# Kernel optimization log

Measured on AMD Instinct MI355X. Metric: run time of the kernel, lower is better.

The kernel has to match this reference:

```python
import jax, jax.numpy as jnp
import numpy as np
import math

N_HEAD = 8
LN_EPS = 1e-5


def _layernorm(x, w, b):
    # Biased variance as in the triton kernel: var = E[x^2] - mean^2
    mean = jnp.mean(x, axis=-1, keepdims=True)
    var = jnp.mean(x * x, axis=-1, keepdims=True) - mean * mean
    return (x - mean) * jax.lax.rsqrt(var + LN_EPS) * w + b


def _gelu_tanh(x):
    # matches triton gelu: tanh approximation
    return 0.5 * x * (1.0 + jnp.tanh(0.7978845608 * (x + 0.044715 * x * x * x)))


def _causal_attention(qkv, n_head):
    B, T, C3 = qkv.shape
    C = C3 // 3
    D = C // n_head
    q, k, v = jnp.split(qkv, 3, axis=-1)
    q = q.reshape(B, T, n_head, D)
    k = k.reshape(B, T, n_head, D)
    v = v.reshape(B, T, n_head, D)
    scale = 1.0 / math.sqrt(D)
    scores = jnp.einsum('bqhd,bkhd->bhqk', q, k) * scale  # [B,H,T,T]
    causal = jnp.tril(jnp.ones((T, T), dtype=bool))
    scores = jnp.where(causal, scores, -jnp.inf)
    p = jax.nn.softmax(scores, axis=-1)
    out = jnp.einsum('bhqk,bkhd->bqhd', p, v)
    return out.reshape(B, T, C)


def setup_inputs() -> dict:
    key = jax.random.key(0)
    ks = jax.random.split(key, 8)
    B, T, C = 8, 2048, 768
    s = 0.02
    return {
        'x': jax.random.normal(ks[0], (B, T, C), jnp.float32),
        'ln1_w': jnp.ones((C,), jnp.float32),
        'ln1_b': jnp.zeros((C,), jnp.float32),
        'w_qkv': jax.random.normal(ks[1], (3 * C, C), jnp.float32) * s,
        'b_qkv': jnp.zeros((3 * C,), jnp.float32),
        'w_attn_proj': jax.random.normal(ks[2], (C, C), jnp.float32) * s,
        'b_attn_proj': jnp.zeros((C,), jnp.float32),
        'ln2_w': jnp.ones((C,), jnp.float32),
        'ln2_b': jnp.zeros((C,), jnp.float32),
        'w_fc': jax.random.normal(ks[3], (4 * C, C), jnp.float32) * s,
        'b_fc': jnp.zeros((4 * C,), jnp.float32),
        'w_mlp_proj': jax.random.normal(ks[4], (C, 4 * C), jnp.float32) * s,
        'b_mlp_proj': jnp.zeros((C,), jnp.float32),
    }


def reference(x, ln1_w, ln1_b, w_qkv, b_qkv, w_attn_proj, b_attn_proj,
              ln2_w, ln2_b, w_fc, b_fc, w_mlp_proj, b_mlp_proj):
    # attention block: fused LN + QKV linear, causal flash attention, out proj, residual
    qkv = _layernorm(x, ln1_w, ln1_b) @ w_qkv.T + b_qkv          # [B,T,3C]
    att = _causal_attention(qkv, N_HEAD)                          # [B,T,C]
    x = x + (att @ w_attn_proj.T + b_attn_proj)
    # MLP block: fused LN + fc + gelu, proj, residual
    h = _gelu_tanh(_layernorm(x, ln2_w, ln2_b) @ w_fc.T + b_fc)   # [B,T,4C]
    x = x + (h @ w_mlp_proj.T + b_mlp_proj)
    return x
```

## Files before the change

kernel.cpp:

```cpp
#include <hip/hip_runtime.h>
#include <hip/hip_bf16.h>
#include <cstdint>
#include <cstddef>

typedef __attribute__((ext_vector_type(8))) short bf16x8;
typedef __attribute__((ext_vector_type(4))) short bf16x4;
typedef __attribute__((ext_vector_type(4))) float f32x4;
typedef __attribute__((ext_vector_type(16))) float f32x16;

#define GLB_AS(p) ((const __attribute__((address_space(1))) void*)(p))
#define LDS_AS(p) ((__attribute__((address_space(3))) void*)(p))

__device__ __forceinline__ short f2bf(float f) {
    union { float f; unsigned u; } x; x.f = f;
    unsigned r = (x.u + 0x7fffu + ((x.u >> 16) & 1u)) >> 16;
    return (short)r;
}
__device__ __forceinline__ unsigned packbf2(float a, float b) {
    union { float f; unsigned u; } x, y; x.f = a; y.f = b;
    return (x.u >> 16) | (y.u & 0xffff0000u);
}
__device__ __forceinline__ f32x4 MF(bf16x8 a, bf16x8 b, f32x4 c) {
    return __builtin_amdgcn_mfma_f32_16x16x32_bf16(a, b, c, 0, 0, 0);
}
__device__ __forceinline__ f32x16 MF32(bf16x8 a, bf16x8 b, f32x16 c) {
    return __builtin_amdgcn_mfma_f32_32x32x16_bf16(a, b, c, 0, 0, 0);
}

__global__ __launch_bounds__(256) void k_cast4(const float* __restrict__ s0,
                                               const float* __restrict__ s1,
                                               const float* __restrict__ s2,
                                               const float* __restrict__ s3,
                                               short* __restrict__ d0,
                                               short* __restrict__ d1,
                                               short* __restrict__ d2,
                                               short* __restrict__ d3,
                                               int n0, int n1, int n2, int n3) {
    const int total = n0 + n1 + n2 + n3;
    int i = blockIdx.x * 256 + threadIdx.x;
    const int stride = gridDim.x * 256;
    for (; i < total; i += stride) {
        int j = i;
        const float* s; short* d;
        if (j < n0) { s = s0; d = d0; }
        else {
            j -= n0;
            if (j < n1) { s = s1; d = d1; }
            else {
                j -= n1;
                if (j < n2) { s = s2; d = d2; }
                else { j -= n2; s = s3; d = d3; }
            }
        }
        float4 v = ((const float4*)s)[j];
        bf16x4 o;
        o[0] = f2bf(v.x); o[1] = f2bf(v.y); o[2] = f2bf(v.z); o[3] = f2bf(v.w);
        ((bf16x4*)d)[j] = o;
    }
}

__global__ __launch_bounds__(256) void k_layernorm(const float* __restrict__ x,
                                                   const float* __restrict__ w,
                                                   const float* __restrict__ b,
                                                   short* __restrict__ out) {
    const int row = blockIdx.x;
    const int tid = threadIdx.x;
    const float* xr = x + (size_t)row * 768;
    float v0 = xr[tid], v1 = xr[tid + 256], v2 = xr[tid + 512];
    float s = v0 + v1 + v2;
    float ss = v0 * v0 + v1 * v1 + v2 * v2;
    #pragma unroll
    for (int m = 32; m; m >>= 1) { s += __shfl_xor(s, m); ss += __shfl_xor(ss, m); }
    __shared__ float red[8];
    int wid = tid >> 6, lane = tid & 63;
    if (lane == 0) { red[wid] = s; red[4 + wid] = ss; }
    __syncthreads();
    s = red[0] + red[1] + red[2] + red[3];
    ss = red[4] + red[5] + red[6] + red[7];
    float mean = s * (1.f / 768.f);
    float var = ss * (1.f / 768.f) - mean * mean;
    float inv = rsqrtf(var + 1e-5f);
    short* orow = out + (size_t)row * 768;
    orow[tid]       = f2bf((v0 - mean) * inv * w[tid]       + b[tid]);
    orow[tid + 256] = f2bf((v1 - mean) * inv * w[tid + 256] + b[tid + 256]);
    orow[tid + 512] = f2bf((v2 - mean) * inv * w[tid + 512] + b[tid + 512]);
}

template <int EPI, int NFR>
__global__ __launch_bounds__(512, 2) void k_gemm256(const short* __restrict__ A,
                                                    const short* __restrict__ B,
                                                    const float* __restrict__ bias,
                                                    const float* __restrict__ res,
                                                    void* __restrict__ out,
                                                    int M, int N, int K) {
    __shared__ short As2[2][256 * 64];
    __shared__ short Bs2[2][NFR * 64 * 64];
    const int tid = threadIdx.x, lane = tid & 63, wid = tid >> 6;
    const int l4 = lane & 15, lh = lane >> 4;
    const int wm = wid >> 2, wn = wid & 3;
    const int gx = gridDim.x;
    const int nwg = gx * gridDim.y;
    int wg = blockIdx.y * gx + blockIdx.x;
    { const int q = nwg >> 3; wg = (wg & 7) * q + (wg >> 3); }
    const int row0 = (wg / gx) * 256, col0 = (wg % gx) * (NFR * 64);

    auto stageA = [&](short* lds, int mh, int k0) {
        #pragma unroll
        for (int i = 0; i < 2; ++i) {
            const int chunk = wid * 2 + i;
            const int dl = mh * 16384 + chunk * 1024 + lane * 16;
            const int r = dl >> 7;
            const int cb = (dl & 127) ^ ((r & 7) << 4);
            __builtin_amdgcn_global_load_lds(
                GLB_AS(A + (size_t)(row0 + r) * K + k0 + (cb >> 1)),
                LDS_AS(lds + mh * 8192 + chunk * 512), 16, 0, 0);
        }
    };
    auto stageB = [&](short* lds, int k0) {
        #pragma unroll
        for (int i = 0; i < NFR; ++i) {
            const int chunk = wid * NFR + i;
            const int dl = chunk * 1024 + lane * 16;
            const int r = dl >> 7;
            const int cb = (dl & 127) ^ ((r & 7) << 4);
            __builtin_amdgcn_global_load_lds(
                GLB_AS(B + (size_t)(col0 + r) * K + k0 + (cb >> 1)),
                LDS_AS(lds + chunk * 512), 16, 0, 0);
        }
    };
    auto rd = [&](const short* lds, int r, int kb) -> bf16x8 {
        return *(const bf16x8*)((const char*)lds + r * 128 +
                                ((kb * 64 + lh * 16) ^ ((r & 7) << 4)));
    };

    f32x4 acc[8][NFR] = {};
    bf16x8 a[4][2], b0[2][2], b1[2][2];
    const int NT = K >> 6;

    stageA(As2[0], 0, 0);
    stageA(As2[0], 1, 0);
    stageB(Bs2[0], 0);
    asm volatile("s_waitcnt vmcnt(0)" ::: "memory");
    __builtin_amdgcn_s_barrier();

    for (int t = 0; t < NT; ++t) {
        const int cur = t & 1, nxt = cur ^ 1;
        const short* Ac = As2[cur];
        const short* Bc = Bs2[cur];
        const int kn = (t + 1) << 6;
        const bool more = (t + 1 < NT);
        #pragma unroll
        for (int mi = 0; mi < 4; ++mi) {
            const int r = wm * 128 + mi * 16 + l4;
            a[mi][0] = rd(Ac, r, 0); a[mi][1] = rd(Ac, r, 1);
        }
        #pragma unroll
        for (int ni = 0; ni < 2; ++ni) {
            const int r = wn * (NFR * 16) + ni * 16 + l4;
            b0[ni][0] = rd(Bc, r, 0); b0[ni][1] = rd(Bc, r, 1);
        }
        if (more) { stageA(As2[nxt], 0, kn); stageA(As2[nxt], 1, kn); }
        __builtin_amdgcn_s_setprio(1);
        #pragma unroll
        for (int mi = 0; mi < 4; ++mi)
            #pragma unroll
            for (int ni = 0; ni < 2; ++ni) {
                acc[mi][ni] = MF(a[mi][0], b0[ni][0], acc[mi][ni]);
                acc[mi][ni] = MF(a[mi][1], b0[ni][1], acc[mi][ni]);
            }
        __builtin_amdgcn_s_setprio(0);
        __builtin_amdgcn_s_barrier();
        #pragma unroll
        for (int j = 0; j < NFR - 2; ++j) {
            const int r = wn * (NFR * 16) + (2 + j) * 16 + l4;
            b1[j][0] = rd(Bc, r, 0); b1[j][1] = rd(Bc, r, 1);
        }
        if (more) stageB(Bs2[nxt], kn);
        __builtin_amdgcn_s_setprio(1);
        #pragma unroll
        for (int mi = 0; mi < 4; ++mi)
            #pragma unroll
            for (int j = 0; j < NFR - 2; ++j) {
                acc[mi][2 + j] = MF(a[mi][0], b1[j][0], acc[mi][2 + j]);
                acc[mi][2 + j] = MF(a[mi][1], b1[j][1], acc[mi][2 + j]);
            }
        __builtin_amdgcn_s_setprio(0);
        __builtin_amdgcn_s_barrier();
        #pragma unroll
        for (int mi = 0; mi < 4; ++mi) {
            const int r = wm * 128 + (4 + mi) * 16 + l4;
            a[mi][0] = rd(Ac, r, 0); a[mi][1] = rd(Ac, r, 1);
        }
        __builtin_amdgcn_s_setprio(1);
        #pragma unroll
        for (int mi = 0; mi < 4; ++mi)
            #pragma unroll
            for (int j = 0; j < NFR - 2; ++j) {
                acc[4 + mi][2 + j] = MF(a[mi][0], b1[j][0], acc[4 + mi][2 + j]);
                acc[4 + mi][2 + j] = MF(a[mi][1], b1[j][1], acc[4 + mi][2 + j]);
            }
        __builtin_amdgcn_s_setprio(0);
        __builtin_amdgcn_s_barrier();
        __builtin_amdgcn_s_setprio(1);
        #pragma unroll
        for (int mi = 0; mi < 4; ++mi)
            #pragma unroll
            for (int ni = 0; ni < 2; ++ni) {
                acc[4 + mi][ni] = MF(a[mi][0], b0[ni][0], acc[4 + mi][ni]);
                acc[4 + mi][ni] = MF(a[mi][1], b0[ni][1], acc[4 + mi][ni]);
            }
        __builtin_amdgcn_s_setprio(0);
        asm volatile("s_waitcnt vmcnt(0)" ::: "memory");
        __builtin_amdgcn_s_barrier();
    }

    #pragma unroll
    for (int mi = 0; mi < 8; ++mi) {
        const int rowb = row0 + wm * 128 + mi * 16 + lh * 4;
        #pragma unroll
        for (int ni = 0; ni < NFR; ++ni) {
            const int col = col0 + wn * (NFR * 16) + ni * 16 + l4;
            const float bv = bias[col];
            #pragma unroll
            for (int j = 0; j < 4; ++j) {
                const size_t idx = (size_t)(rowb + j) * N + col;
                float v = acc[mi][ni][j] + bv;
                if (EPI == 0) {
                    ((short*)out)[idx] = f2bf(v);
                } else if (EPI == 1) {
                    ((float*)out)[idx] = v + res[idx];
                } else {
                    float u = v + 0.044715f * v * v * v;
                    float t = 1.f - 2.f / (__expf(1.5957691216f * u) + 1.f);
                    ((short*)out)[idx] = f2bf(0.5f * v * (1.f + t));
                }
            }
        }
    }
}

__global__ __launch_bounds__(256, 2) void k_attn6(const short* __restrict__ qkv,
                                                  short* __restrict__ att) {
    __shared__ short Ks[2][64 * 128];
    __shared__ short Vs[2][96 * 64];
    const int tid = threadIdx.x, lane = tid & 63, wid = tid >> 6;
    const int lq = lane & 31, hi = lane >> 5;
    const int h = blockIdx.y, b = blockIdx.z;
    const short* base = qkv + (size_t)b * 2048 * 2304 + h * 96;
    const short* Kb = base + 768;
    const short* Vb = base + 1536;
    const int vkvr = (tid / 12) * 4, vd0 = (tid % 12) * 8;
    const int vslot = (vkvr & ~12) | ((vkvr & 4) << 1) | ((vkvr & 8) >> 1);
    bf16x8 vreg[4];
    const float QSC = 0.14724445f;

    auto stageK = [&](int jt, int bb) {
        const int kv0 = jt * 64;
        for (int c = wid; c < 16; c += 4) {
            const int dl = c * 1024 + lane * 16;
            const int row = dl >> 8;
            const int scol = (dl & 255) ^ ((row & 7) << 4);
            __builtin_amdgcn_global_load_lds(GLB_AS(Kb + (size_t)(kv0 + row) * 2304 + (scol >> 1)),
                                             LDS_AS(&Ks[bb][c * 512]), 16, 0, 0);
        }
    };
    auto loadV = [&](int jt) {
        if (tid < 192) {
            const int kv0 = jt * 64;
            #pragma unroll
            for (int e = 0; e < 4; ++e)
                vreg[e] = *(const bf16x8*)(Vb + (size_t)(kv0 + vkvr + e) * 2304 + vd0);
        }
    };
    auto writeV = [&](int bb) {
        if (tid < 192) {
            #pragma unroll
            for (int f = 0; f < 8; ++f) {
                const int row = vd0 + f;
                const int sw = ((row & 7) ^ ((row >> 3) & 7)) << 4;
                const int byte = (row * 128 + vslot * 2) ^ sw;
                bf16x4 w4;
                w4[0] = vreg[0][f]; w4[1] = vreg[1][f]; w4[2] = vreg[2][f]; w4[3] = vreg[3][f];
                *(bf16x4*)((char*)&Vs[bb][0] + byte) = w4;
            }
        }
    };

    for (int half = 0; half < 2; ++half) {
        const int qt = half ? 15 - (int)blockIdx.x : (int)blockIdx.x;
        const int q0 = qt * 128 + wid * 32;
        const int qa = q0 + lq;

        bf16x8 qf[6];
        #pragma unroll
        for (int kb = 0; kb < 6; ++kb) {
            bf16x8 v = *(const bf16x8*)(base + (size_t)qa * 2304 + kb * 16 + hi * 8);
            #pragma unroll
            for (int e = 0; e < 8; ++e) {
                union { unsigned u; float f; } x;
                x.u = ((unsigned)(unsigned short)v[e]) << 16;
                qf[kb][e] = f2bf(x.f * QSC);
            }
        }

        f32x16 o[3] = {};
        float lrow = 0.f;
        const int nt = 2 * qt + 2;

        stageK(0, 0);
        loadV(0);
        asm volatile("s_waitcnt vmcnt(0)" ::: "memory");
        writeV(0);
        __syncthreads();

        int cur = 0;
        for (int jt = 0; jt < nt; ++jt) {
            const int nxt = cur ^ 1;
            const bool more = (jt + 1 < nt);
            if (more) { stageK(jt + 1, nxt); loadV(jt + 1); }

            const int kv0 = jt * 64;
            if (kv0 <= q0 + 31) {
                const bool full = (kv0 + 63 <= q0);
                f32x16 s0 = {}, s1 = {};
                #pragma unroll
                for (int kb = 0; kb < 6; ++kb) {
                    const int r0 = lq, r1 = 32 + lq;
                    bf16x8 kf0 = *(const bf16x8*)((const char*)&Ks[cur][0] +
                                  r0 * 256 + ((kb * 32 + hi * 16) ^ ((r0 & 7) << 4)));
                    bf16x8 kf1 = *(const bf16x8*)((const char*)&Ks[cur][0] +
                                  r1 * 256 + ((kb * 32 + hi * 16) ^ ((r1 & 7) << 4)));
                    s0 = MF32(kf0, qf[kb], s0);
                    s1 = MF32(kf1, qf[kb], s1);
                }
                if (!full) {
                    #pragma unroll
                    for (int r = 0; r < 16; ++r) {
                        const int kvl = (r & 3) + 8 * (r >> 2) + 4 * hi;
                        if (kv0 + kvl > qa) s0[r] = -INFINITY;
                        if (kv0 + 32 + kvl > qa) s1[r] = -INFINITY;
                    }
                }
                #pragma unroll
                for (int r = 0; r < 16; ++r) {
                    s0[r] = exp2f(s0[r]);
                    s1[r] = exp2f(s1[r]);
                }
                float ar[16];
                #pragma unroll
                for (int r = 0; r < 16; ++r) ar[r] = s0[r] + s1[r];
                #pragma unroll
                for (int st = 8; st; st >>= 1)
                    #pragma unroll
                    for (int r = 0; r < 8; ++r)
                        if (r < st) ar[r] += ar[r + st];
                lrow += ar[0] + __shfl_xor(ar[0], 32);
                unsigned pk0[8], pk1[8];
                #pragma unroll
                for (int j = 0; j < 8; ++j) {
                    pk0[j] = packbf2(s0[2 * j], s0[2 * j + 1]);
                    pk1[j] = packbf2(s1[2 * j], s1[2 * j + 1]);
                }
                #pragma unroll
                for (int db = 0; db < 3; ++db) {
                    const int vrow = db * 32 + lq;
                    const int vsw = ((vrow & 7) ^ ((vrow >> 3) & 7)) << 4;
                    #pragma unroll
                    for (int c = 0; c < 4; ++c) {
                        bf16x8 vf = *(const bf16x8*)((const char*)&Vs[cur][0] +
                                     vrow * 128 + ((c * 32 + hi * 16) ^ vsw));
                        union { unsigned u[4]; bf16x8 v; } pa;
                        const unsigned* pk = (c < 2) ? pk0 : pk1;
                        const int o4 = (c & 1) * 4;
                        pa.u[0] = pk[o4]; pa.u[1] = pk[o4 + 1];
                        pa.u[2] = pk[o4 + 2]; pa.u[3] = pk[o4 + 3];
                        o[db] = MF32(vf, pa.v, o[db]);
                    }
                }
            }

            if (more) {
                asm volatile("s_waitcnt vmcnt(0)" ::: "memory");
                writeV(nxt);
            }
            __syncthreads();
            cur = nxt;
        }

        const float inv = 1.f / lrow;
        short* orow = att + (size_t)((size_t)b * 2048 + qa) * 768 + h * 96;
        #pragma unroll
        for (int db = 0; db < 3; ++db)
            #pragma unroll
            for (int j = 0; j < 4; ++j) {
                bf16x4 ov;
                #pragma unroll
                for (int e = 0; e < 4; ++e) ov[e] = f2bf(o[db][4 * j + e] * inv);
                *(bf16x4*)(orow + db * 32 + 8 * j + 4 * hi) = ov;
            }
    }
}

extern "C" void kernel_launch(void* const* d_in, const int* in_sizes, int n_in,
                              void* d_out, int out_size, void* d_ws, size_t ws_size,
                              hipStream_t stream) {
    (void)in_sizes; (void)n_in; (void)out_size; (void)ws_size;
    const float* x      = (const float*)d_in[0];
    const float* ln1_w  = (const float*)d_in[1];
    const float* ln1_b  = (const float*)d_in[2];
    const float* w_qkv  = (const float*)d_in[3];
    const float* b_qkv  = (const float*)d_in[4];
    const float* w_proj = (const float*)d_in[5];
    const float* b_proj = (const float*)d_in[6];
    const float* ln2_w  = (const float*)d_in[7];
    const float* ln2_b  = (const float*)d_in[8];
    const float* w_fc   = (const float*)d_in[9];
    const float* b_fc   = (const float*)d_in[10];
    const float* w_mlp  = (const float*)d_in[11];
    const float* b_mlp  = (const float*)d_in[12];

    const int C = 768, M = 8 * 2048;

    char* ws = (char*)d_ws;
    size_t off = 0;
    auto alloc = [&](size_t bytes) {
        char* p = ws + off;
        off += (bytes + 255) & ~(size_t)255;
        return p;
    };
    short* wqkv_b = (short*)alloc((size_t)3 * C * C * 2);
    short* wproj_b = (short*)alloc((size_t)C * C * 2);
    short* wfc_b  = (short*)alloc((size_t)4 * C * C * 2);
    short* wmlp_b = (short*)alloc((size_t)4 * C * C * 2);
    short* bufA   = (short*)alloc((size_t)M * C * 2);
    short* bufB   = (short*)alloc((size_t)M * 4 * C * 2);
    float* x2     = (float*)alloc((size_t)M * C * 4);

    k_cast4<<<dim3(1728), dim3(256), 0, stream>>>(
        w_qkv, w_proj, w_fc, w_mlp, wqkv_b, wproj_b, wfc_b, wmlp_b,
        3 * C * C / 4, C * C / 4, 4 * C * C / 4, 4 * C * C / 4);

    k_layernorm<<<dim3(M), dim3(256), 0, stream>>>(x, ln1_w, ln1_b, bufA);
    k_gemm256<0, 3><<<dim3(2304 / 192, M / 256), dim3(512), 0, stream>>>(
        bufA, wqkv_b, b_qkv, nullptr, bufB, M, 2304, C);
    k_attn6<<<dim3(8, 8, 8), dim3(256), 0, stream>>>(bufB, bufA);
    k_gemm256<1, 3><<<dim3(768 / 192, M / 256), dim3(512), 0, stream>>>(
        bufA, wproj_b, b_proj, x, x2, M, C, C);
    k_layernorm<<<dim3(M), dim3(256), 0, stream>>>(x2, ln2_w, ln2_b, bufA);
    k_gemm256<2, 4><<<dim3(3072 / 256, M / 256), dim3(512), 0, stream>>>(
        bufA, wfc_b, b_fc, nullptr, bufB, M, 3072, C);
    k_gemm256<1, 3><<<dim3(768 / 192, M / 256), dim3(512), 0, stream>>>(
        bufB, wmlp_b, b_mlp, x2, d_out, M, C, 4 * C);
}
```

Before: 434.8 us.

## Add 32x32 MFMA GEMM for FC, specialize 192-wide GEMM, retune attention grid

```diff
diff --git a/kernel.cpp b/kernel.cpp
--- a/kernel.cpp
+++ b/kernel.cpp
@@ -86,13 +86,14 @@
     orow[tid + 512] = f2bf((v2 - mean) * inv * w[tid + 512] + b[tid + 512]);
 }
 
-template <int EPI, int NFR>
-__global__ __launch_bounds__(512, 2) void k_gemm256(const short* __restrict__ A,
+template <int EPI>
+__global__ __launch_bounds__(512, 2) void k_gemm192(const short* __restrict__ A,
                                                     const short* __restrict__ B,
                                                     const float* __restrict__ bias,
                                                     const float* __restrict__ res,
                                                     void* __restrict__ out,
                                                     int M, int N, int K) {
+    const int NFR = 3;
     __shared__ short As2[2][256 * 64];
     __shared__ short Bs2[2][NFR * 64 * 64];
     const int tid = threadIdx.x, lane = tid & 63, wid = tid >> 6;
@@ -134,7 +135,7 @@
     };
 
     f32x4 acc[8][NFR] = {};
-    bf16x8 a[4][2], b0[2][2], b1[2][2];
+    bf16x8 a[4][2], b0[2][2], b1[1][2];
     const int NT = K >> 6;
 
     stageA(As2[0], 0, 0);
@@ -159,7 +160,11 @@
             const int r = wn * (NFR * 16) + ni * 16 + l4;
             b0[ni][0] = rd(Bc, r, 0); b0[ni][1] = rd(Bc, r, 1);
         }
-        if (more) { stageA(As2[nxt], 0, kn); stageA(As2[nxt], 1, kn); }
+        if (more) {
+            stageA(As2[nxt], 0, kn);
+            stageA(As2[nxt], 1, kn);
+            stageB(Bs2[nxt], kn);
+        }
         __builtin_amdgcn_s_setprio(1);
         #pragma unroll
         for (int mi = 0; mi < 4; ++mi)
@@ -170,20 +175,16 @@
             }
         __builtin_amdgcn_s_setprio(0);
         __builtin_amdgcn_s_barrier();
-        #pragma unroll
-        for (int j = 0; j < NFR - 2; ++j) {
-            const int r = wn * (NFR * 16) + (2 + j) * 16 + l4;
-            b1[j][0] = rd(Bc, r, 0); b1[j][1] = rd(Bc, r, 1);
-        }
-        if (more) stageB(Bs2[nxt], kn);
-        __builtin_amdgcn_s_setprio(1);
-        #pragma unroll
-        for (int mi = 0; mi < 4; ++mi)
-            #pragma unroll
-            for (int j = 0; j < NFR - 2; ++j) {
-                acc[mi][2 + j] = MF(a[mi][0], b1[j][0], acc[mi][2 + j]);
-                acc[mi][2 + j] = MF(a[mi][1], b1[j][1], acc[mi][2 + j]);
-            }
+        {
+            const int r = wn * (NFR * 16) + 2 * 16 + l4;
+            b1[0][0] = rd(Bc, r, 0); b1[0][1] = rd(Bc, r, 1);
+        }
+        __builtin_amdgcn_s_setprio(1);
+        #pragma unroll
+        for (int mi = 0; mi < 4; ++mi) {
+            acc[mi][2] = MF(a[mi][0], b1[0][0], acc[mi][2]);
+            acc[mi][2] = MF(a[mi][1], b1[0][1], acc[mi][2]);
+        }
         __builtin_amdgcn_s_setprio(0);
         __builtin_amdgcn_s_barrier();
         #pragma unroll
@@ -193,12 +194,10 @@
         }
         __builtin_amdgcn_s_setprio(1);
         #pragma unroll
-        for (int mi = 0; mi < 4; ++mi)
-            #pragma unroll
-            for (int j = 0; j < NFR - 2; ++j) {
-                acc[4 + mi][2 + j] = MF(a[mi][0], b1[j][0], acc[4 + mi][2 + j]);
-                acc[4 + mi][2 + j] = MF(a[mi][1], b1[j][1], acc[4 + mi][2 + j]);
-            }
+        for (int mi = 0; mi < 4; ++mi) {
+            acc[4 + mi][2] = MF(a[mi][0], b1[0][0], acc[4 + mi][2]);
+            acc[4 + mi][2] = MF(a[mi][1], b1[0][1], acc[4 + mi][2]);
+        }
         __builtin_amdgcn_s_setprio(0);
         __builtin_amdgcn_s_barrier();
         __builtin_amdgcn_s_setprio(1);
@@ -239,13 +238,146 @@
     }
 }
 
-__global__ __launch_bounds__(256, 2) void k_attn6(const short* __restrict__ qkv,
+template <int EPI>
+__global__ __launch_bounds__(512, 2) void k_gemm32t(const short* __restrict__ A,
+                                                    const short* __restrict__ B,
+                                                    const float* __restrict__ bias,
+                                                    const float* __restrict__ res,
+                                                    void* __restrict__ out,
+                                                    int M, int N, int K) {
+    __shared__ short As2[2][256 * 64];
+    __shared__ short Bs2[2][256 * 64];
+    const int tid = threadIdx.x, lane = tid & 63, wid = tid >> 6;
+    const int lq = lane & 31, hi = lane >> 5;
+    const int wm = wid >> 2, wn = wid & 3;
+    const int gx = gridDim.x;
+    const int nwg = gx * gridDim.y;
+    int wg = blockIdx.y * gx + blockIdx.x;
+    { const int q = nwg >> 3; wg = (wg & 7) * q + (wg >> 3); }
+    const int row0 = (wg / gx) * 256, col0 = (wg % gx) * 256;
+
+    auto stage = [&](const short* __restrict__ src, int base_row, short* lds,
+                     int mh, int k0) {
+        #pragma unroll
+        for (int i = 0; i < 2; ++i) {
+            const int chunk = wid * 2 + i;
+            const int dl = mh * 16384 + chunk * 1024 + lane * 16;
+            const int r = dl >> 7;
+            const int cb = (dl & 127) ^ ((r & 7) << 4);
+            __builtin_amdgcn_global_load_lds(
+                GLB_AS(src + (size_t)(base_row + r) * K + k0 + (cb >> 1)),
+                LDS_AS(lds + mh * 8192 + chunk * 512), 16, 0, 0);
+        }
+    };
+    auto rd32 = [&](const short* lds, int r, int kb) -> bf16x8 {
+        return *(const bf16x8*)((const char*)lds + r * 128 +
+                                ((kb * 32 + hi * 16) ^ ((r & 7) << 4)));
+    };
+
+    f32x16 acc[4][2] = {};
+    bf16x8 a[2][4], b0[4], b1[4];
+    const int NT = K >> 6;
+
+    stage(A, row0, As2[0], 0, 0);
+    stage(A, row0, As2[0], 1, 0);
+    stage(B, col0, Bs2[0], 0, 0);
+    stage(B, col0, Bs2[0], 1, 0);
+    asm volatile("s_waitcnt vmcnt(0)" ::: "memory");
+    __builtin_amdgcn_s_barrier();
+
+    for (int t = 0; t < NT; ++t) {
+        const int cur = t & 1, nxt = cur ^ 1;
+        const short* Ac = As2[cur];
+        const short* Bc = Bs2[cur];
+        const int kn = (t + 1) << 6;
+        const bool more = (t + 1 < NT);
+        #pragma unroll
+        for (int rt = 0; rt < 2; ++rt)
+            #pragma unroll
+            for (int k = 0; k < 4; ++k)
+                a[rt][k] = rd32(Ac, wm * 128 + rt * 32 + lq, k);
+        #pragma unroll
+        for (int k = 0; k < 4; ++k) b0[k] = rd32(Bc, wn * 64 + lq, k);
+        if (more) {
+            stage(A, row0, As2[nxt], 0, kn);
+            stage(A, row0, As2[nxt], 1, kn);
+            stage(B, col0, Bs2[nxt], 0, kn);
+            stage(B, col0, Bs2[nxt], 1, kn);
+        }
+        __builtin_amdgcn_s_setprio(1);
+        #pragma unroll
+        for (int rt = 0; rt < 2; ++rt)
+            #pragma unroll
+            for (int k = 0; k < 4; ++k)
+                acc[rt][0] = MF32(a[rt][k], b0[k], acc[rt][0]);
+        __builtin_amdgcn_s_setprio(0);
+        __builtin_amdgcn_s_barrier();
+        #pragma unroll
+        for (int k = 0; k < 4; ++k) b1[k] = rd32(Bc, wn * 64 + 32 + lq, k);
+        __builtin_amdgcn_s_setprio(1);
+        #pragma unroll
+        for (int rt = 0; rt < 2; ++rt)
+            #pragma unroll
+            for (int k = 0; k < 4; ++k)
+                acc[rt][1] = MF32(a[rt][k], b1[k], acc[rt][1]);
+        __builtin_amdgcn_s_setprio(0);
+        __builtin_amdgcn_s_barrier();
+        #pragma unroll
+        for (int rt = 0; rt < 2; ++rt)
+            #pragma unroll
+            for (int k = 0; k < 4; ++k)
+                a[rt][k] = rd32(Ac, wm * 128 + (2 + rt) * 32 + lq, k);
+        __builtin_amdgcn_s_setprio(1);
+        #pragma unroll
+        for (int rt = 0; rt < 2; ++rt)
+            #pragma unroll
+            for (int k = 0; k < 4; ++k)
+                acc[2 + rt][1] = MF32(a[rt][k], b1[k], acc[2 + rt][1]);
+        __builtin_amdgcn_s_setprio(0);
+        __builtin_amdgcn_s_barrier();
+        __builtin_amdgcn_s_setprio(1);
+        #pragma unroll
+        for (int rt = 0; rt < 2; ++rt)
+            #pragma unroll
+            for (int k = 0; k < 4; ++k)
+                acc[2 + rt][0] = MF32(a[rt][k], b0[k], acc[2 + rt][0]);
+        __builtin_amdgcn_s_setprio(0);
+        asm volatile("s_waitcnt vmcnt(0)" ::: "memory");
+        __builtin_amdgcn_s_barrier();
+    }
+
+    #pragma unroll
+    for (int rt = 0; rt < 4; ++rt)
+        #pragma unroll
+        for (int ct = 0; ct < 2; ++ct) {
+            const int col = col0 + wn * 64 + ct * 32 + lq;
+            const float bv = bias[col];
+            #pragma unroll
+            for (int j = 0; j < 16; ++j) {
+                const int row = row0 + wm * 128 + rt * 32 + (j & 3) + 8 * (j >> 2) + 4 * hi;
+                const size_t idx = (size_t)row * N + col;
+                float v = acc[rt][ct][j] + bv;
+                if (EPI == 0) {
+                    ((short*)out)[idx] = f2bf(v);
+                } else if (EPI == 1) {
+                    ((float*)out)[idx] = v + res[idx];
+                } else {
+                    float u = v + 0.044715f * v * v * v;
+                    float tt = 1.f - 2.f / (__expf(1.5957691216f * u) + 1.f);
+                    ((short*)out)[idx] = f2bf(0.5f * v * (1.f + tt));
+                }
+            }
+        }
+}
+
+__global__ __launch_bounds__(256, 2) void k_attn7(const short* __restrict__ qkv,
                                                   short* __restrict__ att) {
     __shared__ short Ks[2][64 * 128];
     __shared__ short Vs[2][96 * 64];
     const int tid = threadIdx.x, lane = tid & 63, wid = tid >> 6;
     const int lq = lane & 31, hi = lane >> 5;
-    const int h = blockIdx.y, b = blockIdx.z;
+    const int L = blockIdx.x;
+    const int h = L & 7, bx = (L >> 3) & 7, b = L >> 6;
     const short* base = qkv + (size_t)b * 2048 * 2304 + h * 96;
     const short* Kb = base + 768;
     const short* Vb = base + 1536;
@@ -287,7 +419,7 @@
     };
 
     for (int half = 0; half < 2; ++half) {
-        const int qt = half ? 15 - (int)blockIdx.x : (int)blockIdx.x;
+        const int qt = half ? 15 - bx : bx;
         const int q0 = qt * 128 + wid * 32;
         const int qa = q0 + lq;
 
@@ -323,6 +455,7 @@
             if (kv0 <= q0 + 31) {
                 const bool full = (kv0 + 63 <= q0);
                 f32x16 s0 = {}, s1 = {};
+                __builtin_amdgcn_s_setprio(1);
                 #pragma unroll
                 for (int kb = 0; kb < 6; ++kb) {
                     const int r0 = lq, r1 = 32 + lq;
@@ -333,6 +466,7 @@
                     s0 = MF32(kf0, qf[kb], s0);
                     s1 = MF32(kf1, qf[kb], s1);
                 }
+                __builtin_amdgcn_s_setprio(0);
                 if (!full) {
                     #pragma unroll
                     for (int r = 0; r < 16; ++r) {
@@ -361,6 +495,7 @@
                     pk0[j] = packbf2(s0[2 * j], s0[2 * j + 1]);
                     pk1[j] = packbf2(s1[2 * j], s1[2 * j + 1]);
                 }
+                __builtin_amdgcn_s_setprio(1);
                 #pragma unroll
                 for (int db = 0; db < 3; ++db) {
                     const int vrow = db * 32 + lq;
@@ -377,6 +512,7 @@
                         o[db] = MF32(vf, pa.v, o[db]);
                     }
                 }
+                __builtin_amdgcn_s_setprio(0);
             }
 
             if (more) {
@@ -441,14 +577,14 @@
         3 * C * C / 4, C * C / 4, 4 * C * C / 4, 4 * C * C / 4);
 
     k_layernorm<<<dim3(M), dim3(256), 0, stream>>>(x, ln1_w, ln1_b, bufA);
-    k_gemm256<0, 3><<<dim3(2304 / 192, M / 256), dim3(512), 0, stream>>>(
+    k_gemm192<0><<<dim3(2304 / 192, M / 256), dim3(512), 0, stream>>>(
         bufA, wqkv_b, b_qkv, nullptr, bufB, M, 2304, C);
-    k_attn6<<<dim3(8, 8, 8), dim3(256), 0, stream>>>(bufB, bufA);
-    k_gemm256<1, 3><<<dim3(768 / 192, M / 256), dim3(512), 0, stream>>>(
+    k_attn7<<<dim3(512), dim3(256), 0, stream>>>(bufB, bufA);
+    k_gemm192<1><<<dim3(768 / 192, M / 256), dim3(512), 0, stream>>>(
         bufA, wproj_b, b_proj, x, x2, M, C, C);
     k_layernorm<<<dim3(M), dim3(256), 0, stream>>>(x2, ln2_w, ln2_b, bufA);
-    k_gemm256<2, 4><<<dim3(3072 / 256, M / 256), dim3(512), 0, stream>>>(
+    k_gemm32t<2><<<dim3(3072 / 256, M / 256), dim3(512), 0, stream>>>(
         bufA, wfc_b, b_fc, nullptr, bufB, M, 3072, C);
-    k_gemm256<1, 3><<<dim3(768 / 192, M / 256), dim3(512), 0, stream>>>(
+    k_gemm192<1><<<dim3(768 / 192, M / 256), dim3(512), 0, stream>>>(
         bufB, wmlp_b, b_mlp, x2, d_out, M, C, 4 * C);
 }
```

After: 443.4 us. No clear change (+2.0%).
